# Kernel optimization log

Hardware: AMD Instinct MI355X
Metric: run time of the kernel (lower is better)

## Reference

```python
import jax, jax.numpy as jnp
import numpy as np

H = 14
N = H * H
DIM = 768
INT = 5
LAM = 3.5


def fft_conv_grouped(x, w):
    # x: (B, g*in_c, N) real; w: (g, int_c, in_c, H, H//2+1) complex
    g, int_c, in_c = w.shape[:3]
    B = x.shape[0]
    xf = jnp.fft.rfftn(x.reshape(B, g, in_c, H, H), axes=(-2, -1), norm='ortho')
    yf = jnp.einsum('bgchf,gichf->bgihf', xf, w)
    y = jnp.fft.irfftn(yf, s=(H, H), axes=(-2, -1), norm='ortho')
    return y.reshape(B, g * int_c, N)


def soft(x, t):
    # sign(x) * relu(|x| - t)
    return jnp.sign(x) * jnp.maximum(jnp.abs(x) - t, 0.0)


def batch_norm(x, gamma, beta, eps=1e-5):
    # training-mode BatchNorm1d applied per channel over (B, N); x: (B, N, C)
    m = x.mean(axis=(0, 1))
    v = x.var(axis=(0, 1))
    return (x - m) * jax.lax.rsqrt(v + eps) * gamma + beta


def setup_inputs() -> dict:
    key = jax.random.key(0)
    ks = jax.random.split(key, 8)
    B = 32
    Hf = H // 2 + 1
    # kernel: init randn*0.06, then normalize_parameters()
    kr = jax.random.normal(ks[0], (DIM, INT, 1, H, Hf, 2), dtype=jnp.float32) * 0.06
    kc = kr[..., 0] + 1j * kr[..., 1]
    nrm = jnp.sqrt((jnp.abs(kc) ** 2).sum(axis=(2, 3, 4), keepdims=True) * 2.0 / H ** 2)
    kc = kc / nrm
    kernel = jnp.stack([jnp.real(kc), jnp.imag(kc)], axis=-1)
    # L buffer: update_L(lam=1) -> per-group max singular value of Gram kk
    kk = jnp.einsum('gichf,gjchf->gijhf', kc, jnp.conj(kc))
    sv = np.linalg.svd(np.asarray(jnp.transpose(kk, (0, 3, 4, 1, 2))), compute_uv=False)
    L = jnp.asarray(sv.reshape(DIM, -1).max(axis=-1), dtype=jnp.float32)
    hid = 4 * DIM
    return {
        'x': jax.random.normal(ks[1], (B, N, DIM), dtype=jnp.float32),
        'v_w': jax.random.normal(ks[2], (DIM, DIM), dtype=jnp.float32) * 0.02,
        'proj_w': jax.random.normal(ks[3], (DIM, DIM), dtype=jnp.float32) * 0.02,
        'proj_b': jnp.zeros((DIM,), dtype=jnp.float32),
        'kernel': kernel,
        'kernel2': jax.random.normal(ks[4], (DIM, 1, 1, H, Hf, 2), dtype=jnp.float32) * 0.02,
        'n1_g': jnp.ones((DIM,), dtype=jnp.float32),
        'n1_b': jnp.zeros((DIM,), dtype=jnp.float32),
        'n2_g': jnp.ones((DIM,), dtype=jnp.float32),
        'n2_b': jnp.zeros((DIM,), dtype=jnp.float32),
        'fc1_w': jax.random.normal(ks[5], (hid, DIM), dtype=jnp.float32) * 0.02,
        'fc1_b': jnp.zeros((hid,), dtype=jnp.float32),
        'fc2_w': jax.random.normal(ks[6], (DIM, hid), dtype=jnp.float32) * 0.02,
        'fc2_b': jnp.zeros((DIM,), dtype=jnp.float32),
        'L': L,
    }


def reference(x, v_w, proj_w, proj_b, kernel, kernel2, n1_g, n1_b, n2_g, n2_b, fc1_w, fc1_b, fc2_w, fc2_b, L):
    k = kernel[..., 0] + 1j * kernel[..., 1]                 # (g, int, 1, H, Hf)
    kk = jnp.einsum('gichf,gjchf->gijhf', k, jnp.conj(k))     # (g, int, int, H, Hf)
    vx = x @ v_w.T                                            # v Linear, no bias
    xc = jnp.swapaxes(vx, -2, -1)                             # (B, C, N)
    u = fft_conv_grouped(xc, k)                               # (B, g*int, N)
    Lv = jnp.repeat(L, INT)[None, :, None]                    # (1, g*int, 1)
    # ISTA: init soft-threshold then 3 gradient + shrink steps
    s = soft(u, LAM)
    for _ in range(3):
        s = s - (fft_conv_grouped(s, kk) - u) / Lv
        s = soft(s, LAM / Lv)
    # reconstruct with conjugate-transposed kernel, then mix with kernel2
    new = fft_conv_grouped(s, jnp.swapaxes(jnp.conj(k), 1, 2))  # (B, g, N)
    k2 = kernel2[..., 0] + 1j * kernel2[..., 1]
    new = fft_conv_grouped(new, k2)
    new = jnp.swapaxes(new, -2, -1)                           # (B, N, C)
    new = x + (batch_norm(new, n1_g, n1_b) @ proj_w.T + proj_b)
    h = jax.nn.gelu(batch_norm(new, n2_g, n2_b) @ fc1_w.T + fc1_b, approximate=False)
    return new + (h @ fc2_w.T + fc2_b)
```

## Files before the change

kernel.cpp:

```cpp
#include <hip/hip_runtime.h>
#include <cmath>

typedef unsigned short u16;
typedef __bf16 bf16x8 __attribute__((ext_vector_type(8)));
typedef float f32x4 __attribute__((ext_vector_type(4)));
typedef float float4v __attribute__((ext_vector_type(4)));
typedef u16 ushort4v __attribute__((ext_vector_type(4)));
typedef u16 ushort8v __attribute__((ext_vector_type(8)));

#define DIMC 768
#define NP 196
#define MTOT 6272
#define HIDC 3072
#define LAMC 3.5f

__device__ const float C14d[14] = {
  1.0f, 0.9009688679024191f, 0.6234898018587336f, 0.22252093395631445f,
  -0.22252093395631445f, -0.6234898018587336f, -0.9009688679024191f, -1.0f,
  -0.9009688679024191f, -0.6234898018587336f, -0.22252093395631445f,
  0.22252093395631445f, 0.6234898018587336f, 0.9009688679024191f
};
__device__ const float S14d[14] = {
  0.0f, 0.43388373911755823f, 0.7818314824680298f, 0.9749279121818236f,
  0.9749279121818236f, 0.7818314824680298f, 0.43388373911755823f, 0.0f,
  -0.43388373911755823f, -0.7818314824680298f, -0.9749279121818236f,
  -0.9749279121818236f, -0.7818314824680298f, -0.43388373911755823f
};

__device__ __forceinline__ u16 f2bf(float f) {
  unsigned u = __builtin_bit_cast(unsigned, f);
  unsigned r = u + 0x7FFFu + ((u >> 16) & 1u);
  return (u16)(r >> 16);
}

typedef const __attribute__((address_space(1))) u16* gas_p;
typedef __attribute__((address_space(3))) u16* las_p;
__device__ __forceinline__ void gl16(const u16* g, u16* l) {
  __builtin_amdgcn_global_load_lds((gas_p)g, (las_p)l, 16, 0, 0);
}

__global__ __launch_bounds__(256) void initfg_k(u16* __restrict__ Ff, u16* __restrict__ Gf) {
  int idx = blockIdx.x * 256 + threadIdx.x;
  if (idx < 50176) {
    int j = idx & 7, lane = (idx >> 3) & 63;
    int mk = idx >> 9, k0 = mk % 7, m0 = mk / 7;
    int s = m0 * 16 + (lane & 15);
    int q = k0 * 32 + (lane >> 4) * 8 + j;
    float v = 0.f;
    if (q < 196) {
      int kr = s >> 4, f = (s >> 1) & 7, r = q / 14, c = q % 14;
      int th = (kr * r + f * c) % 14;
      v = (s & 1) ? -S14d[th] : C14d[th];
    }
    Ff[idx] = f2bf(v);
  } else if (idx < 50176 + 46592) {
    int t = idx - 50176;
    int j = t & 7, lane = (t >> 3) & 63;
    int pk = t >> 9, k0 = pk % 7, p0 = pk / 7;
    int p = p0 * 16 + (lane & 15);
    int s = k0 * 32 + (lane >> 4) * 8 + j;
    float v = 0.f;
    if (p < 196) {
      int kr = s >> 4, f = (s >> 1) & 7, r = p / 14, c = p % 14;
      int th = (kr * r + f * c) % 14;
      float w = (f == 0 || f == 7) ? 1.f : 2.f;
      v = (w * (1.f / 196.f)) * ((s & 1) ? -S14d[th] : C14d[th]);
    }
    Gf[t] = f2bf(v);
  }
}

__global__ __launch_bounds__(256) void cvtw2_k(
    const float* __restrict__ w0, const float* __restrict__ w1,
    u16* __restrict__ o0, u16* __restrict__ o1) {
  int idx = blockIdx.x * 256 + threadIdx.x;
  const float* s; u16* d; int base;
  if (idx < 147456) { s = w0; d = o0; base = 0; }
  else              { s = w1; d = o1; base = 147456; }
  int i4 = (idx - base) * 4;
  float4v v = *(const float4v*)(s + i4);
  ushort4v o;
#pragma unroll
  for (int j = 0; j < 4; ++j) o[j] = f2bf(v[j]);
  *(ushort4v*)(d + i4) = o;
}

__global__ __launch_bounds__(256) void cvt4_k(const float* __restrict__ s,
                                              u16* __restrict__ d, int n4) {
  int idx = blockIdx.x * 256 + threadIdx.x;
  if (idx >= n4) return;
  int i4 = idx * 4;
  float4v v = *(const float4v*)(s + i4);
  ushort4v o;
#pragma unroll
  for (int j = 0; j < 4; ++j) o[j] = f2bf(v[j]);
  *(ushort4v*)(d + i4) = o;
}

__global__ __launch_bounds__(256) void scalefc1_k(const float* __restrict__ w,
    const float* __restrict__ sc, u16* __restrict__ d) {
  int idx = blockIdx.x * 256 + threadIdx.x;
  int i4 = idx * 4;
  int k = i4 % DIMC;
  float4v v = *(const float4v*)(w + i4);
  float4v s = *(const float4v*)(sc + k);
  v = v * s;
  ushort4v o;
#pragma unroll
  for (int j = 0; j < 4; ++j) o[j] = f2bf(v[j]);
  *(ushort4v*)(d + i4) = o;
}

__global__ __launch_bounds__(256) void c0_k(const float* __restrict__ projw,
    const float* __restrict__ sh, const float* __restrict__ pb,
    float* __restrict__ c0) {
  int n = blockIdx.x * 256 + threadIdx.x;
  if (n >= DIMC) return;
  const float* row = projw + (size_t)n * DIMC;
  float s = 0.f;
  for (int g = 0; g < DIMC; g += 4) {
    float4v r = *(const float4v*)(row + g);
    float4v h = *(const float4v*)(sh + g);
    s += r[0] * h[0] + r[1] * h[1] + r[2] * h[2] + r[3] * h[3];
  }
  c0[n] = s + pb[n];
}

__global__ __launch_bounds__(256) void d0_k(const float* __restrict__ fc1w,
    const float* __restrict__ sh, const float* __restrict__ fb,
    float* __restrict__ d0) {
  int n = blockIdx.x * 256 + threadIdx.x;
  if (n >= HIDC) return;
  const float* row = fc1w + (size_t)n * DIMC;
  float s = 0.f;
  for (int k = 0; k < DIMC; k += 4) {
    float4v r = *(const float4v*)(row + k);
    float4v h = *(const float4v*)(sh + k);
    s += r[0] * h[0] + r[1] * h[1] + r[2] * h[2] + r[3] * h[3];
  }
  d0[n] = s + fb[n];
}

__global__ __launch_bounds__(256) void base_k(const float* __restrict__ x,
    const float* __restrict__ c0, float* __restrict__ new2,
    u16* __restrict__ new2bf) {
  int idx = blockIdx.x * 256 + threadIdx.x;
  size_t i4 = (size_t)idx * 4;
  int c = (int)(i4 % DIMC);
  float4v v = *(const float4v*)(x + i4);
  float4v a = *(const float4v*)(c0 + c);
  v = v + a;
  *(float4v*)(new2 + i4) = v;
  ushort4v o;
#pragma unroll
  for (int j = 0; j < 4; ++j) o[j] = f2bf(v[j]);
  *(ushort4v*)(new2bf + i4) = o;
}

__global__ __launch_bounds__(64) void tilesum_k(const int* __restrict__ cnt,
    const int* __restrict__ wl, const float* __restrict__ newm,
    float* __restrict__ tsum, float* __restrict__ tsq,
    unsigned* __restrict__ maskg, unsigned* __restrict__ bmask) {
  const int nf = *cnt;
  const int lane = threadIdx.x;
  for (int wi = blockIdx.x; wi < nf; wi += gridDim.x) {
    int tile = wl[wi];
    int g = tile >> 5, b = tile & 31;
    float s = 0.f, q = 0.f;
    for (int m = lane; m < 196; m += 64) {
      float v = newm[((size_t)b * 196 + m) * DIMC + g];
      s += v; q += v * v;
    }
#pragma unroll
    for (int off = 32; off; off >>= 1) { s += __shfl_xor(s, off); q += __shfl_xor(q, off); }
    if (lane == 0) {
      tsum[tile] = s; tsq[tile] = q;
      atomicOr(&maskg[g], 1u << b);
      atomicOr(bmask, 1u << b);
    }
  }
}

__global__ __launch_bounds__(256) void stats1_fin_k(const float* __restrict__ tsum,
    const float* __restrict__ tsq, const unsigned* __restrict__ maskg,
    const float* __restrict__ gam, const float* __restrict__ bet,
    float* __restrict__ scale, float* __restrict__ shift) {
  int c = blockIdx.x * 256 + threadIdx.x;
  if (c >= DIMC) return;
  unsigned mask = maskg[c];
  float S = 0.f, Q = 0.f;
  for (int b = 0; b < 32; ++b)
    if ((mask >> b) & 1) { S += tsum[c * 32 + b]; Q += tsq[c * 32 + b]; }
  float m = S * (1.0f / 6272.0f);
  float v = Q * (1.0f / 6272.0f) - m * m;
  v = fmaxf(v, 0.f);
  float rs = rsqrtf(v + 1e-5f);
  float sc = gam[c] * rs;
  scale[c] = sc;
  shift[c] = bet[c] - m * sc;
}

__global__ __launch_bounds__(256) void corr_k(const unsigned* __restrict__ maskg,
    const unsigned* __restrict__ bmask, const float* __restrict__ newm,
    const float* __restrict__ projw, const float* __restrict__ sc1,
    float* __restrict__ new2, u16* __restrict__ new2bf) {
  const int b = blockIdx.x, t = threadIdx.x;
  if (!((*bmask >> b) & 1)) return;
  __shared__ int gl[768];
  __shared__ int ngs;
  if (t == 0) {
    int n = 0;
    for (int g = 0; g < DIMC; ++g) if ((maskg[g] >> b) & 1) gl[n++] = g;
    ngs = n;
  }
  __syncthreads();
  const int n_g = ngs;
  for (int m = 0; m < 196; ++m) {
    size_t row = ((size_t)b * 196 + m) * DIMC;
    for (int n = t; n < DIMC; n += 256) {
      float a = 0.f;
      for (int i = 0; i < n_g; ++i) {
        int g = gl[i];
        a += sc1[g] * newm[row + g] * projw[(size_t)n * DIMC + g];
      }
      float nv = new2[row + n] + a;
      new2[row + n] = nv;
      new2bf[row + n] = f2bf(nv);
    }
  }
}

template<int EPI>
__global__ __launch_bounds__(256) void gemm_k(
    const u16* __restrict__ A, const u16* __restrict__ Bw,
    const float* __restrict__ bias, const float* __restrict__ res,
    void* __restrict__ Cp, int Nr, int Kr, int ld, int NB) {
  __shared__ __attribute__((aligned(16))) u16 As[128 * 32];
  __shared__ __attribute__((aligned(16))) u16 Bs[128 * 32];
  const int t = threadIdx.x;
  const int wid = t >> 6, lane = t & 63;

  const int bid = blockIdx.x;
  const int xcd = bid & 7, j = bid >> 3;
  const int bmi = xcd + 8 * (j / NB);
  if (bmi >= 49) return;
  const int bn = (j % NB) * 128, bm = bmi * 128;

  const int wm = (wid >> 1) * 64, wn = (wid & 1) * 64;
  const int l15 = lane & 15, l4 = lane >> 4;
  const int srow = lane >> 2, scol = (lane & 3) * 8;

  f32x4 acc[4][4];
#pragma unroll
  for (int a = 0; a < 4; ++a)
#pragma unroll
    for (int b2 = 0; b2 < 4; ++b2) acc[a][b2] = (f32x4){0.f, 0.f, 0.f, 0.f};

  const u16* gA0 = A + (size_t)(bm + wid * 16 + srow) * ld + scol;
  const u16* gB0 = Bw + (size_t)(bn + wid * 16 + srow) * ld + scol;
  u16* lA = As + wid * 512;
  u16* lB = Bs + wid * 512;

  for (int k0 = 0; k0 < Kr; k0 += 32) {
    gl16(gA0 + k0, lA);
    gl16(gA0 + (size_t)64 * ld + k0, lA + 2048);
    gl16(gB0 + k0, lB);
    gl16(gB0 + (size_t)64 * ld + k0, lB + 2048);
    __syncthreads();

    bf16x8 af[4], bfv[4];
#pragma unroll
    for (int mb = 0; mb < 4; ++mb)
      af[mb] = *(const bf16x8*)&As[(wm + mb * 16 + l15) * 32 + l4 * 8];
#pragma unroll
    for (int nb = 0; nb < 4; ++nb)
      bfv[nb] = *(const bf16x8*)&Bs[(wn + nb * 16 + l15) * 32 + l4 * 8];
#pragma unroll
    for (int mb = 0; mb < 4; ++mb)
#pragma unroll
      for (int nb = 0; nb < 4; ++nb)
        acc[mb][nb] = __builtin_amdgcn_mfma_f32_16x16x32_bf16(af[mb], bfv[nb], acc[mb][nb], 0, 0, 0);
    __syncthreads();
  }

#pragma unroll
  for (int mb = 0; mb < 4; ++mb) {
#pragma unroll
    for (int nb = 0; nb < 4; ++nb) {
      int n = bn + wn + nb * 16 + l15;
      if (EPI == 0) {
        int m0 = bm + wm + mb * 16 + l4 * 4;
        int bb = m0 / 196, np0 = m0 - bb * 196;
        *(float4v*)&((float*)Cp)[((size_t)bb * DIMC + n) * 196 + np0] =
            (float4v){acc[mb][nb][0], acc[mb][nb][1], acc[mb][nb][2], acc[mb][nb][3]};
      } else {
#pragma unroll
        for (int r = 0; r < 4; ++r) {
          int m = bm + wm + mb * 16 + l4 * 4 + r;
          float v = acc[mb][nb][r];
          if (EPI == 1) {
            ((float*)Cp)[(size_t)m * Nr + n] = v + bias[n] + res[(size_t)m * Nr + n];
          } else {
            float vb = v + bias[n];
            float ge = 0.5f * vb * (1.f + erff(vb * 0.70710678118654752f));
            ((u16*)Cp)[(size_t)m * Nr + n] = f2bf(ge);
          }
        }
      }
    }
  }
}

__global__ __launch_bounds__(256) void stats_part_k(const float* __restrict__ A,
                                                    float* __restrict__ part) {
  int blk = blockIdx.x, t = threadIdx.x;
  float s0a = 0, s0b = 0, s0c = 0, s1a = 0, s1b = 0, s1c = 0;
  const float* base = A + (size_t)blk * 64 * DIMC;
  for (int r = 0; r < 64; ++r) {
    const float* row = base + (size_t)r * DIMC;
    float v0 = row[t], v1 = row[t + 256], v2 = row[t + 512];
    s0a += v0; s1a += v0 * v0;
    s0b += v1; s1b += v1 * v1;
    s0c += v2; s1c += v2 * v2;
  }
  part[(size_t)blk * DIMC + t] = s0a;
  part[(size_t)blk * DIMC + t + 256] = s0b;
  part[(size_t)blk * DIMC + t + 512] = s0c;
  float* p2 = part + 98 * DIMC;
  p2[(size_t)blk * DIMC + t] = s1a;
  p2[(size_t)blk * DIMC + t + 256] = s1b;
  p2[(size_t)blk * DIMC + t + 512] = s1c;
}

__global__ __launch_bounds__(256) void stats_fin_k(const float* __restrict__ part,
    const float* __restrict__ gam, const float* __restrict__ bet,
    float* __restrict__ scale, float* __restrict__ shift) {
  int c = blockIdx.x * 256 + threadIdx.x;
  if (c >= DIMC) return;
  float S = 0.f, Q = 0.f;
  for (int b = 0; b < 98; ++b) {
    S += part[(size_t)b * DIMC + c];
    Q += part[(size_t)(98 + b) * DIMC + c];
  }
  float m = S * (1.0f / 6272.0f);
  float v = Q * (1.0f / 6272.0f) - m * m;
  v = fmaxf(v, 0.f);
  float rs = rsqrtf(v + 1e-5f);
  float sc = gam[c] * rs;
  scale[c] = sc;
  shift[c] = bet[c] - m * sc;
}

__global__ __launch_bounds__(64) void checkmfma_k(
    const float* __restrict__ vxt, const float* __restrict__ kern,
    const u16* __restrict__ Ff, const u16* __restrict__ Gf,
    int* __restrict__ cnt, int* __restrict__ wl) {
  __shared__ float xf[16 * 228];
  const int lane = threadIdx.x;
  const int wgb = blockIdx.x;
  const int g = wgb >> 1, bhalf = wgb & 1;
  const int tl = lane & 15, h = lane >> 4;
  const float* xbase = vxt + ((size_t)(bhalf * 16 + tl) * DIMC + g) * 196;

  bf16x8 Bx[7];
#pragma unroll
  for (int k0 = 0; k0 < 7; ++k0) {
    int q0 = k0 * 32 + h * 8;
    ushort8v tv;
    if (k0 < 6) {
      float4v f0 = *(const float4v*)(xbase + q0);
      float4v f1 = *(const float4v*)(xbase + q0 + 4);
#pragma unroll
      for (int j = 0; j < 4; ++j) { tv[j] = f2bf(f0[j]); tv[j + 4] = f2bf(f1[j]); }
    } else {
#pragma unroll
      for (int j = 0; j < 8; ++j) {
        int q = q0 + j;
        tv[j] = (q < 196) ? f2bf(xbase[q]) : (u16)0;
      }
    }
    Bx[k0] = __builtin_bit_cast(bf16x8, tv);
  }

  for (int m0 = 0; m0 < 14; ++m0) {
    f32x4 acc = (f32x4){0.f, 0.f, 0.f, 0.f};
#pragma unroll
    for (int k0 = 0; k0 < 7; ++k0) {
      bf16x8 Af = __builtin_bit_cast(bf16x8,
          *(const ushort8v*)(Ff + ((size_t)(m0 * 7 + k0) * 64 + lane) * 8));
      acc = __builtin_amdgcn_mfma_f32_16x16x32_bf16(Af, Bx[k0], acc, 0, 0, 0);
    }
    *(f32x4*)&xf[tl * 228 + m0 * 16 + h * 4] = acc;
  }

  bf16x8 By[5][7];
#pragma unroll
  for (int i = 0; i < 5; ++i) {
    const float* kb = kern + ((size_t)g * 5 + i) * 224;
#pragma unroll
    for (int k0 = 0; k0 < 7; ++k0) {
      f32x4 x0 = *(const f32x4*)&xf[tl * 228 + k0 * 32 + h * 8];
      f32x4 x1 = *(const f32x4*)&xf[tl * 228 + k0 * 32 + h * 8 + 4];
      int mb = k0 * 16 + h * 4;
      float2 ka = *(const float2*)(kb + (mb + 0) * 2);
      float2 kc = *(const float2*)(kb + (mb + 1) * 2);
      float2 ke = *(const float2*)(kb + (mb + 2) * 2);
      float2 kg = *(const float2*)(kb + (mb + 3) * 2);
      ushort8v tv;
      tv[0] = f2bf(ka.x * x0[0] - ka.y * x0[1]);
      tv[1] = f2bf(ka.x * x0[1] + ka.y * x0[0]);
      tv[2] = f2bf(kc.x * x0[2] - kc.y * x0[3]);
      tv[3] = f2bf(kc.x * x0[3] + kc.y * x0[2]);
      tv[4] = f2bf(ke.x * x1[0] - ke.y * x1[1]);
      tv[5] = f2bf(ke.x * x1[1] + ke.y * x1[0]);
      tv[6] = f2bf(kg.x * x1[2] - kg.y * x1[3]);
      tv[7] = f2bf(kg.x * x1[3] + kg.y * x1[2]);
      By[i][k0] = __builtin_bit_cast(bf16x8, tv);
    }
  }

  float vmax = 0.f;
  for (int p0 = 0; p0 < 13; ++p0) {
    f32x4 a0 = (f32x4){0.f, 0.f, 0.f, 0.f};
    f32x4 a1 = a0, a2 = a0, a3 = a0, a4 = a0;
#pragma unroll
    for (int k0 = 0; k0 < 7; ++k0) {
      bf16x8 Ag = __builtin_bit_cast(bf16x8,
          *(const ushort8v*)(Gf + ((size_t)(p0 * 7 + k0) * 64 + lane) * 8));
      a0 = __builtin_amdgcn_mfma_f32_16x16x32_bf16(Ag, By[0][k0], a0, 0, 0, 0);
      a1 = __builtin_amdgcn_mfma_f32_16x16x32_bf16(Ag, By[1][k0], a1, 0, 0, 0);
      a2 = __builtin_amdgcn_mfma_f32_16x16x32_bf16(Ag, By[2][k0], a2, 0, 0, 0);
      a3 = __builtin_amdgcn_mfma_f32_16x16x32_bf16(Ag, By[3][k0], a3, 0, 0, 0);
      a4 = __builtin_amdgcn_mfma_f32_16x16x32_bf16(Ag, By[4][k0], a4, 0, 0, 0);
    }
#pragma unroll
    for (int r = 0; r < 4; ++r) {
      vmax = fmaxf(vmax, fabsf(a0[r]));
      vmax = fmaxf(vmax, fabsf(a1[r]));
      vmax = fmaxf(vmax, fabsf(a2[r]));
      vmax = fmaxf(vmax, fabsf(a3[r]));
      vmax = fmaxf(vmax, fabsf(a4[r]));
    }
  }
  vmax = fmaxf(vmax, __shfl_xor(vmax, 16));
  vmax = fmaxf(vmax, __shfl_xor(vmax, 32));
  if (lane < 16 && vmax > (LAMC - 0.1f)) {
    int idx = atomicAdd(cnt, 1);
    wl[idx] = g * 32 + bhalf * 16 + lane;
  }
}

__global__ __launch_bounds__(64) void slow_k(
    const float* __restrict__ vxt, const float* __restrict__ kern,
    const float* __restrict__ kern2, const float* __restrict__ Lbuf,
    const int* __restrict__ cnt, const int* __restrict__ wl,
    float* __restrict__ outp) {
  const int t = threadIdx.x;
  __shared__ float TC[196], TSn[196];
  __shared__ float xs[196];
  __shared__ float t1R[112], t1I[112];
  __shared__ float t2R[112], t2I[112];
  __shared__ float zr[112], zi[112];
  __shared__ float kR[5][112], kI[5][112];
  __shared__ float uu[5][196];
  __shared__ float ss[5][196];
  __shared__ float k2R[112], k2I[112];

  for (int i = t; i < 196; i += 64) {
    int a = i / 14, c = i - (i / 14) * 14;
    int m = (a * c) % 14;
    TC[i] = C14d[m]; TSn[i] = S14d[m];
  }
  const int ntile = *cnt;

  auto rowsFwd = [&](const float* xsrc) {
    for (int i = t; i < 112; i += 64) {
      int r = i >> 3, f = i & 7;
      const float* xp = xsrc + r * 14;
      const float* tc = &TC[f * 14]; const float* tsn = &TSn[f * 14];
      float ar = 0.f, ai = 0.f;
#pragma unroll
      for (int c = 0; c < 14; ++c) { float xv = xp[c]; ar += xv * tc[c]; ai -= xv * tsn[c]; }
      t1R[i] = ar; t1I[i] = ai;
    }
    __syncthreads();
  };
  auto colsFwd = [&](float* oR, float* oI) {
    for (int i = t; i < 112; i += 64) {
      int kr = i >> 3, f = i & 7;
      const float* tc = &TC[kr * 14]; const float* tsn = &TSn[kr * 14];
      float br = 0.f, bi = 0.f;
#pragma unroll
      for (int r = 0; r < 14; ++r) {
        float xr = t1R[r * 8 + f], xi = t1I[r * 8 + f];
        br += tc[r] * xr + tsn[r] * xi;
        bi += tc[r] * xi - tsn[r] * xr;
      }
      oR[i] = br; oI[i] = bi;
    }
    __syncthreads();
  };
  auto colsInv = [&]() {
    for (int i = t; i < 112; i += 64) {
      int r = i >> 3, f = i & 7;
      const float* tc = &TC[r * 14]; const float* tsn = &TSn[r * 14];
      float br = 0.f, bi = 0.f;
#pragma unroll
      for (int kr = 0; kr < 14; ++kr) {
        float xr = t1R[kr * 8 + f], xi = t1I[kr * 8 + f];
        br += tc[kr] * xr - tsn[kr] * xi;
        bi += tc[kr] * xi + tsn[kr] * xr;
      }
      t2R[i] = br; t2I[i] = bi;
    }
    __syncthreads();
  };
  auto rowVal = [&](int r, int c) -> float {
    const float* pR = &t2R[r * 8]; const float* pI = &t2I[r * 8];
    float v = pR[0] + ((c & 1) ? -pR[7] : pR[7]);
    float s2 = 0.f;
#pragma unroll
    for (int f = 1; f < 7; ++f) s2 += pR[f] * TC[f * 14 + c] - pI[f] * TSn[f * 14 + c];
    return (v + 2.f * s2) * (1.0f / 196.0f);
  };

  for (int widx = blockIdx.x; widx < ntile; widx += gridDim.x) {
    const int tile = wl[widx];
    const int g = tile >> 5, b = tile & 31;
    __syncthreads();
    for (int i = t; i < 560; i += 64) {
      int ii = i / 112, p = i - ii * 112;
      const float* kp = kern + ((size_t)g * 5 + ii) * 224 + p * 2;
      kR[ii][p] = kp[0]; kI[ii][p] = kp[1];
    }
    for (int i = t; i < 196; i += 64) xs[i] = vxt[((size_t)b * DIMC + g) * 196 + i];
    for (int i = t; i < 112; i += 64) {
      k2R[i] = kern2[(size_t)g * 224 + i * 2];
      k2I[i] = kern2[(size_t)g * 224 + i * 2 + 1];
    }
    __syncthreads();

    rowsFwd(xs);
    colsFwd(zr, zi);
    for (int ii = 0; ii < 5; ++ii) {
      for (int i = t; i < 112; i += 64) {
        float a = kR[ii][i], b2 = kI[ii][i];
        t1R[i] = a * zr[i] - b2 * zi[i];
        t1I[i] = a * zi[i] + b2 * zr[i];
      }
      __syncthreads();
      colsInv();
      for (int i = t; i < 196; i += 64) uu[ii][i] = rowVal(i / 14, i - (i / 14) * 14);
      __syncthreads();
    }

    const float invL = 1.0f / Lbuf[g];
    const float thr = LAMC * invL;
    {
      float* up = &uu[0][0];
      float* sp = &ss[0][0];
      for (int i = t; i < 980; i += 64) {
        float v = up[i];
        float a = fabsf(v) - LAMC;
        sp[i] = a > 0.f ? copysignf(a, v) : 0.f;
      }
    }
    __syncthreads();

    for (int iter = 0; iter < 4; ++iter) {
      for (int i = t; i < 112; i += 64) { zr[i] = 0.f; zi[i] = 0.f; }
      __syncthreads();
      for (int ii = 0; ii < 5; ++ii) {
        rowsFwd(&ss[ii][0]);
        colsFwd(t2R, t2I);
        for (int i = t; i < 112; i += 64) {
          float a = kR[ii][i], b2 = kI[ii][i];
          zr[i] += a * t2R[i] + b2 * t2I[i];
          zi[i] += a * t2I[i] - b2 * t2R[i];
        }
        __syncthreads();
      }
      if (iter == 3) break;
      for (int ii = 0; ii < 5; ++ii) {
        for (int i = t; i < 112; i += 64) {
          float a = kR[ii][i], b2 = kI[ii][i];
          t1R[i] = a * zr[i] - b2 * zi[i];
          t1I[i] = a * zi[i] + b2 * zr[i];
        }
        __syncthreads();
        colsInv();
        for (int i = t; i < 196; i += 64) {
          float v = rowVal(i / 14, i - (i / 14) * 14);
          float sv = ss[ii][i] - (v - uu[ii][i]) * invL;
          float aa = fabsf(sv) - thr;
          ss[ii][i] = aa > 0.f ? copysignf(aa, sv) : 0.f;
        }
        __syncthreads();
      }
    }

    if (t < 28) {
      int kr = t >> 1, f = (t & 1) * 7;
      int d = kr * 8 + f;
      int srci = ((14 - kr) % 14) * 8 + f;
      float pr = 0.5f * (zr[d] + zr[srci]);
      float pi = 0.5f * (zi[d] - zi[srci]);
      zr[d] = pr; zi[d] = pi;
    }
    __syncthreads();
    for (int i = t; i < 112; i += 64) {
      float a = k2R[i], b2 = k2I[i];
      t1R[i] = a * zr[i] - b2 * zi[i];
      t1I[i] = a * zi[i] + b2 * zr[i];
    }
    __syncthreads();
    colsInv();
    for (int i = t; i < 196; i += 64)
      outp[((size_t)(b * 196 + i)) * DIMC + g] = rowVal(i / 14, i - (i / 14) * 14);
  }
}

extern "C" void kernel_launch(void* const* d_in, const int* in_sizes, int n_in,
                              void* d_out, int out_size, void* d_ws, size_t ws_size,
                              hipStream_t stream) {
  (void)in_sizes; (void)n_in; (void)out_size;
  const float* x      = (const float*)d_in[0];
  const float* v_w    = (const float*)d_in[1];
  const float* proj_w = (const float*)d_in[2];
  const float* proj_b = (const float*)d_in[3];
  const float* kern   = (const float*)d_in[4];
  const float* kern2  = (const float*)d_in[5];
  const float* n1g    = (const float*)d_in[6];
  const float* n1b    = (const float*)d_in[7];
  const float* n2g    = (const float*)d_in[8];
  const float* n2b    = (const float*)d_in[9];
  const float* fc1w   = (const float*)d_in[10];
  const float* fc1b   = (const float*)d_in[11];
  const float* fc2w   = (const float*)d_in[12];
  const float* fc2b   = (const float*)d_in[13];
  const float* Lb     = (const float*)d_in[14];
  float* out = (float*)d_out;

  char* ws = (char*)d_ws;
  size_t o = 0;
  auto alloc = [&](size_t bytes) { size_t r = o; o += (bytes + 255) & ~(size_t)255; return r; };
  u16*   vwbf   = (u16*)(ws + alloc(589824 * 2));
  u16*   fc2bf  = (u16*)(ws + alloc(2359296 * 2));
  u16*   fc1s   = (u16*)(ws + alloc(2359296 * 2));
  u16*   Ffb    = (u16*)(ws + alloc(50176 * 2));
  u16*   Gfb    = (u16*)(ws + alloc(46592 * 2));
  float* sc1    = (float*)(ws + alloc(768 * 4));
  float* sh1    = (float*)(ws + alloc(768 * 4));
  float* sc2    = (float*)(ws + alloc(768 * 4));
  float* sh2    = (float*)(ws + alloc(768 * 4));
  float* c0     = (float*)(ws + alloc(768 * 4));
  float* d0     = (float*)(ws + alloc(3072 * 4));
  float* part   = (float*)(ws + alloc(98 * 768 * 2 * 4));
  char*  zblk   = (char*)(ws + alloc(4096));
  int*      cnt   = (int*)zblk;
  unsigned* bmask = (unsigned*)(zblk + 4);
  unsigned* maskg = (unsigned*)(zblk + 8);
  int*   wl     = (int*)(ws + alloc(24576 * 4));
  float* tsum   = (float*)(ws + alloc(24576 * 4));
  float* tsq    = (float*)(ws + alloc(24576 * 4));
  u16*   xbf    = (u16*)(ws + alloc((size_t)MTOT * DIMC * 2));
  u16*   n2bf   = (u16*)(ws + alloc((size_t)MTOT * DIMC * 2));
  float* vxt    = (float*)(ws + alloc((size_t)MTOT * DIMC * 4));
  float* newm   = (float*)(ws + alloc((size_t)MTOT * DIMC * 4));
  float* new2   = (float*)(ws + alloc((size_t)MTOT * DIMC * 4));
  u16*   hbf    = (u16*)vxt;
  if (ws_size < o) return;

  hipMemsetAsync(zblk, 0, 4096, stream);

  initfg_k<<<378, 256, 0, stream>>>(Ffb, Gfb);
  cvtw2_k<<<2880, 256, 0, stream>>>(v_w, fc2w, vwbf, fc2bf);
  cvt4_k<<<4704, 256, 0, stream>>>(x, xbf, 1204224);

  gemm_k<0><<<336, 256, 0, stream>>>(xbf, vwbf, nullptr, nullptr, vxt, DIMC, DIMC, DIMC, 6);
  checkmfma_k<<<1536, 64, 0, stream>>>(vxt, kern, Ffb, Gfb, cnt, wl);
  slow_k<<<1024, 64, 0, stream>>>(vxt, kern, kern2, Lb, cnt, wl, newm);
  tilesum_k<<<256, 64, 0, stream>>>(cnt, wl, newm, tsum, tsq, maskg, bmask);
  stats1_fin_k<<<3, 256, 0, stream>>>(tsum, tsq, maskg, n1g, n1b, sc1, sh1);
  c0_k<<<3, 256, 0, stream>>>(proj_w, sh1, proj_b, c0);
  base_k<<<4704, 256, 0, stream>>>(x, c0, new2, n2bf);
  corr_k<<<32, 256, 0, stream>>>(maskg, bmask, newm, proj_w, sc1, new2, n2bf);
  stats_part_k<<<98, 256, 0, stream>>>(new2, part);
  stats_fin_k<<<3, 256, 0, stream>>>(part, n2g, n2b, sc2, sh2);
  d0_k<<<12, 256, 0, stream>>>(fc1w, sh2, fc1b, d0);
  scalefc1_k<<<2304, 256, 0, stream>>>(fc1w, sc2, fc1s);
  gemm_k<2><<<1344, 256, 0, stream>>>(n2bf, fc1s, d0, nullptr, hbf, HIDC, DIMC, DIMC, 24);
  gemm_k<1><<<336, 256, 0, stream>>>(hbf, fc2bf, fc2b, new2, out, DIMC, HIDC, HIDC, 6);
}
```

Before: 324.2 us.

## Fuse prep, stats, correction and fc1-folding kernels to cut launches

Merges the three conversion/init kernels into one prep kernel and folds the per-tile sum and sum-of-squares into slow_k. It also fuses the BN1 stats with the c0 projection, and the base add with the sparse correction and BN2 partial sums into a 2D-grid kernel. d0 and the fc1 scaling are merged into one kernel. This cuts launch count and drops a full re-read of new2 for statistics, and it replaces the 32-block serial correction kernel with a 896-block version. The cost is a larger partials buffer and a serial 896-term reduction per channel in stats2fin_k.

```diff
diff --git a/kernel.cpp b/kernel.cpp
--- a/kernel.cpp
+++ b/kernel.cpp
@@ -39,194 +39,60 @@
   __builtin_amdgcn_global_load_lds((gas_p)g, (las_p)l, 16, 0, 0);
 }
 
-__global__ __launch_bounds__(256) void initfg_k(u16* __restrict__ Ff, u16* __restrict__ Gf) {
-  int idx = blockIdx.x * 256 + threadIdx.x;
-  if (idx < 50176) {
-    int j = idx & 7, lane = (idx >> 3) & 63;
-    int mk = idx >> 9, k0 = mk % 7, m0 = mk / 7;
-    int s = m0 * 16 + (lane & 15);
-    int q = k0 * 32 + (lane >> 4) * 8 + j;
-    float v = 0.f;
-    if (q < 196) {
-      int kr = s >> 4, f = (s >> 1) & 7, r = q / 14, c = q % 14;
-      int th = (kr * r + f * c) % 14;
-      v = (s & 1) ? -S14d[th] : C14d[th];
-    }
-    Ff[idx] = f2bf(v);
-  } else if (idx < 50176 + 46592) {
-    int t = idx - 50176;
-    int j = t & 7, lane = (t >> 3) & 63;
-    int pk = t >> 9, k0 = pk % 7, p0 = pk / 7;
-    int p = p0 * 16 + (lane & 15);
-    int s = k0 * 32 + (lane >> 4) * 8 + j;
-    float v = 0.f;
-    if (p < 196) {
-      int kr = s >> 4, f = (s >> 1) & 7, r = p / 14, c = p % 14;
-      int th = (kr * r + f * c) % 14;
-      float w = (f == 0 || f == 7) ? 1.f : 2.f;
-      v = (w * (1.f / 196.f)) * ((s & 1) ? -S14d[th] : C14d[th]);
-    }
-    Gf[t] = f2bf(v);
-  }
-}
-
-__global__ __launch_bounds__(256) void cvtw2_k(
-    const float* __restrict__ w0, const float* __restrict__ w1,
-    u16* __restrict__ o0, u16* __restrict__ o1) {
-  int idx = blockIdx.x * 256 + threadIdx.x;
-  const float* s; u16* d; int base;
-  if (idx < 147456) { s = w0; d = o0; base = 0; }
-  else              { s = w1; d = o1; base = 147456; }
-  int i4 = (idx - base) * 4;
-  float4v v = *(const float4v*)(s + i4);
-  ushort4v o;
-#pragma unroll
-  for (int j = 0; j < 4; ++j) o[j] = f2bf(v[j]);
-  *(ushort4v*)(d + i4) = o;
-}
-
-__global__ __launch_bounds__(256) void cvt4_k(const float* __restrict__ s,
-                                              u16* __restrict__ d, int n4) {
-  int idx = blockIdx.x * 256 + threadIdx.x;
-  if (idx >= n4) return;
-  int i4 = idx * 4;
-  float4v v = *(const float4v*)(s + i4);
-  ushort4v o;
-#pragma unroll
-  for (int j = 0; j < 4; ++j) o[j] = f2bf(v[j]);
-  *(ushort4v*)(d + i4) = o;
-}
-
-__global__ __launch_bounds__(256) void scalefc1_k(const float* __restrict__ w,
-    const float* __restrict__ sc, u16* __restrict__ d) {
-  int idx = blockIdx.x * 256 + threadIdx.x;
-  int i4 = idx * 4;
-  int k = i4 % DIMC;
-  float4v v = *(const float4v*)(w + i4);
-  float4v s = *(const float4v*)(sc + k);
-  v = v * s;
-  ushort4v o;
-#pragma unroll
-  for (int j = 0; j < 4; ++j) o[j] = f2bf(v[j]);
-  *(ushort4v*)(d + i4) = o;
-}
-
-__global__ __launch_bounds__(256) void c0_k(const float* __restrict__ projw,
-    const float* __restrict__ sh, const float* __restrict__ pb,
-    float* __restrict__ c0) {
-  int n = blockIdx.x * 256 + threadIdx.x;
-  if (n >= DIMC) return;
-  const float* row = projw + (size_t)n * DIMC;
-  float s = 0.f;
-  for (int g = 0; g < DIMC; g += 4) {
-    float4v r = *(const float4v*)(row + g);
-    float4v h = *(const float4v*)(sh + g);
-    s += r[0] * h[0] + r[1] * h[1] + r[2] * h[2] + r[3] * h[3];
-  }
-  c0[n] = s + pb[n];
-}
-
-__global__ __launch_bounds__(256) void d0_k(const float* __restrict__ fc1w,
-    const float* __restrict__ sh, const float* __restrict__ fb,
-    float* __restrict__ d0) {
-  int n = blockIdx.x * 256 + threadIdx.x;
-  if (n >= HIDC) return;
-  const float* row = fc1w + (size_t)n * DIMC;
-  float s = 0.f;
-  for (int k = 0; k < DIMC; k += 4) {
-    float4v r = *(const float4v*)(row + k);
-    float4v h = *(const float4v*)(sh + k);
-    s += r[0] * h[0] + r[1] * h[1] + r[2] * h[2] + r[3] * h[3];
-  }
-  d0[n] = s + fb[n];
-}
-
-__global__ __launch_bounds__(256) void base_k(const float* __restrict__ x,
-    const float* __restrict__ c0, float* __restrict__ new2,
-    u16* __restrict__ new2bf) {
-  int idx = blockIdx.x * 256 + threadIdx.x;
-  size_t i4 = (size_t)idx * 4;
-  int c = (int)(i4 % DIMC);
-  float4v v = *(const float4v*)(x + i4);
-  float4v a = *(const float4v*)(c0 + c);
-  v = v + a;
-  *(float4v*)(new2 + i4) = v;
-  ushort4v o;
-#pragma unroll
-  for (int j = 0; j < 4; ++j) o[j] = f2bf(v[j]);
-  *(ushort4v*)(new2bf + i4) = o;
-}
-
-__global__ __launch_bounds__(64) void tilesum_k(const int* __restrict__ cnt,
-    const int* __restrict__ wl, const float* __restrict__ newm,
-    float* __restrict__ tsum, float* __restrict__ tsq,
-    unsigned* __restrict__ maskg, unsigned* __restrict__ bmask) {
-  const int nf = *cnt;
-  const int lane = threadIdx.x;
-  for (int wi = blockIdx.x; wi < nf; wi += gridDim.x) {
-    int tile = wl[wi];
-    int g = tile >> 5, b = tile & 31;
-    float s = 0.f, q = 0.f;
-    for (int m = lane; m < 196; m += 64) {
-      float v = newm[((size_t)b * 196 + m) * DIMC + g];
-      s += v; q += v * v;
-    }
-#pragma unroll
-    for (int off = 32; off; off >>= 1) { s += __shfl_xor(s, off); q += __shfl_xor(q, off); }
-    if (lane == 0) {
-      tsum[tile] = s; tsq[tile] = q;
-      atomicOr(&maskg[g], 1u << b);
-      atomicOr(bmask, 1u << b);
-    }
-  }
-}
-
-__global__ __launch_bounds__(256) void stats1_fin_k(const float* __restrict__ tsum,
-    const float* __restrict__ tsq, const unsigned* __restrict__ maskg,
-    const float* __restrict__ gam, const float* __restrict__ bet,
-    float* __restrict__ scale, float* __restrict__ shift) {
-  int c = blockIdx.x * 256 + threadIdx.x;
-  if (c >= DIMC) return;
-  unsigned mask = maskg[c];
-  float S = 0.f, Q = 0.f;
-  for (int b = 0; b < 32; ++b)
-    if ((mask >> b) & 1) { S += tsum[c * 32 + b]; Q += tsq[c * 32 + b]; }
-  float m = S * (1.0f / 6272.0f);
-  float v = Q * (1.0f / 6272.0f) - m * m;
-  v = fmaxf(v, 0.f);
-  float rs = rsqrtf(v + 1e-5f);
-  float sc = gam[c] * rs;
-  scale[c] = sc;
-  shift[c] = bet[c] - m * sc;
-}
-
-__global__ __launch_bounds__(256) void corr_k(const unsigned* __restrict__ maskg,
-    const unsigned* __restrict__ bmask, const float* __restrict__ newm,
-    const float* __restrict__ projw, const float* __restrict__ sc1,
-    float* __restrict__ new2, u16* __restrict__ new2bf) {
-  const int b = blockIdx.x, t = threadIdx.x;
-  if (!((*bmask >> b) & 1)) return;
-  __shared__ int gl[768];
-  __shared__ int ngs;
-  if (t == 0) {
-    int n = 0;
-    for (int g = 0; g < DIMC; ++g) if ((maskg[g] >> b) & 1) gl[n++] = g;
-    ngs = n;
-  }
-  __syncthreads();
-  const int n_g = ngs;
-  for (int m = 0; m < 196; ++m) {
-    size_t row = ((size_t)b * 196 + m) * DIMC;
-    for (int n = t; n < DIMC; n += 256) {
-      float a = 0.f;
-      for (int i = 0; i < n_g; ++i) {
-        int g = gl[i];
-        a += sc1[g] * newm[row + g] * projw[(size_t)n * DIMC + g];
-      }
-      float nv = new2[row + n] + a;
-      new2[row + n] = nv;
-      new2bf[row + n] = f2bf(nv);
-    }
+__global__ __launch_bounds__(256) void prep_k(
+    const float* __restrict__ v_w, const float* __restrict__ fc2w,
+    const float* __restrict__ x,
+    u16* __restrict__ vwbf, u16* __restrict__ fc2bf, u16* __restrict__ xbf,
+    u16* __restrict__ Ff, u16* __restrict__ Gf) {
+  const int bid = blockIdx.x, t = threadIdx.x;
+  if (bid < 378) {
+    int idx = bid * 256 + t;
+    if (idx < 50176) {
+      int j = idx & 7, lane = (idx >> 3) & 63;
+      int mk = idx >> 9, k0 = mk % 7, m0 = mk / 7;
+      int s = m0 * 16 + (lane & 15);
+      int q = k0 * 32 + (lane >> 4) * 8 + j;
+      float v = 0.f;
+      if (q < 196) {
+        int kr = s >> 4, f = (s >> 1) & 7, r = q / 14, c = q % 14;
+        int th = (kr * r + f * c) % 14;
+        v = (s & 1) ? -S14d[th] : C14d[th];
+      }
+      Ff[idx] = f2bf(v);
+    } else {
+      int t2 = idx - 50176;
+      int j = t2 & 7, lane = (t2 >> 3) & 63;
+      int pk = t2 >> 9, k0 = pk % 7, p0 = pk / 7;
+      int p = p0 * 16 + (lane & 15);
+      int s = k0 * 32 + (lane >> 4) * 8 + j;
+      float v = 0.f;
+      if (p < 196) {
+        int kr = s >> 4, f = (s >> 1) & 7, r = p / 14, c = p % 14;
+        int th = (kr * r + f * c) % 14;
+        float w = (f == 0 || f == 7) ? 1.f : 2.f;
+        v = (w * (1.f / 196.f)) * ((s & 1) ? -S14d[th] : C14d[th]);
+      }
+      Gf[t2] = f2bf(v);
+    }
+  } else if (bid < 3258) {
+    int idx = (bid - 378) * 256 + t;
+    const float* s; u16* d; int base;
+    if (idx < 147456) { s = v_w; d = vwbf; base = 0; }
+    else              { s = fc2w; d = fc2bf; base = 147456; }
+    int i4 = (idx - base) * 4;
+    float4v v = *(const float4v*)(s + i4);
+    ushort4v o;
+#pragma unroll
+    for (int j = 0; j < 4; ++j) o[j] = f2bf(v[j]);
+    *(ushort4v*)(d + i4) = o;
+  } else {
+    int idx = (bid - 3258) * 256 + t;
+    int i4 = idx * 4;
+    float4v v = *(const float4v*)(x + i4);
+    ushort4v o;
+#pragma unroll
+    for (int j = 0; j < 4; ++j) o[j] = f2bf(v[j]);
+    *(ushort4v*)(xbf + i4) = o;
   }
 }
 
@@ -309,46 +175,6 @@
       }
     }
   }
-}
-
-__global__ __launch_bounds__(256) void stats_part_k(const float* __restrict__ A,
-                                                    float* __restrict__ part) {
-  int blk = blockIdx.x, t = threadIdx.x;
-  float s0a = 0, s0b = 0, s0c = 0, s1a = 0, s1b = 0, s1c = 0;
-  const float* base = A + (size_t)blk * 64 * DIMC;
-  for (int r = 0; r < 64; ++r) {
-    const float* row = base + (size_t)r * DIMC;
-    float v0 = row[t], v1 = row[t + 256], v2 = row[t + 512];
-    s0a += v0; s1a += v0 * v0;
-    s0b += v1; s1b += v1 * v1;
-    s0c += v2; s1c += v2 * v2;
-  }
-  part[(size_t)blk * DIMC + t] = s0a;
-  part[(size_t)blk * DIMC + t + 256] = s0b;
-  part[(size_t)blk * DIMC + t + 512] = s0c;
-  float* p2 = part + 98 * DIMC;
-  p2[(size_t)blk * DIMC + t] = s1a;
-  p2[(size_t)blk * DIMC + t + 256] = s1b;
-  p2[(size_t)blk * DIMC + t + 512] = s1c;
-}
-
-__global__ __launch_bounds__(256) void stats_fin_k(const float* __restrict__ part,
-    const float* __restrict__ gam, const float* __restrict__ bet,
-    float* __restrict__ scale, float* __restrict__ shift) {
-  int c = blockIdx.x * 256 + threadIdx.x;
-  if (c >= DIMC) return;
-  float S = 0.f, Q = 0.f;
-  for (int b = 0; b < 98; ++b) {
-    S += part[(size_t)b * DIMC + c];
-    Q += part[(size_t)(98 + b) * DIMC + c];
-  }
-  float m = S * (1.0f / 6272.0f);
-  float v = Q * (1.0f / 6272.0f) - m * m;
-  v = fmaxf(v, 0.f);
-  float rs = rsqrtf(v + 1e-5f);
-  float sc = gam[c] * rs;
-  scale[c] = sc;
-  shift[c] = bet[c] - m * sc;
 }
 
 __global__ __launch_bounds__(64) void checkmfma_k(
@@ -454,7 +280,11 @@
     const float* __restrict__ vxt, const float* __restrict__ kern,
     const float* __restrict__ kern2, const float* __restrict__ Lbuf,
     const int* __restrict__ cnt, const int* __restrict__ wl,
-    float* __restrict__ outp) {
+    float* __restrict__ outp,
+    float* __restrict__ tsum, float* __restrict__ tsq,
+    unsigned* __restrict__ maskg, unsigned* __restrict__ bmask) {
+  const int ntile = *cnt;
+  if ((int)blockIdx.x >= ntile) return;
   const int t = threadIdx.x;
   __shared__ float TC[196], TSn[196];
   __shared__ float xs[196];
@@ -471,7 +301,6 @@
     int m = (a * c) % 14;
     TC[i] = C14d[m]; TSn[i] = S14d[m];
   }
-  const int ntile = *cnt;
 
   auto rowsFwd = [&](const float* xsrc) {
     for (int i = t; i < 112; i += 64) {
@@ -615,8 +444,150 @@
     }
     __syncthreads();
     colsInv();
-    for (int i = t; i < 196; i += 64)
-      outp[((size_t)(b * 196 + i)) * DIMC + g] = rowVal(i / 14, i - (i / 14) * 14);
+    float sacc = 0.f, qacc = 0.f;
+    for (int i = t; i < 196; i += 64) {
+      float v = rowVal(i / 14, i - (i / 14) * 14);
+      outp[((size_t)(b * 196 + i)) * DIMC + g] = v;
+      sacc += v; qacc += v * v;
+    }
+#pragma unroll
+    for (int off = 32; off; off >>= 1) {
+      sacc += __shfl_xor(sacc, off);
+      qacc += __shfl_xor(qacc, off);
+    }
+    if (t == 0) {
+      tsum[tile] = sacc; tsq[tile] = qacc;
+      atomicOr(&maskg[g], 1u << b);
+      atomicOr(bmask, 1u << b);
+    }
+  }
+}
+
+__global__ __launch_bounds__(256) void stats1c0_k(
+    const float* __restrict__ tsum, const float* __restrict__ tsq,
+    const unsigned* __restrict__ maskg,
+    const float* __restrict__ gam, const float* __restrict__ bet,
+    const float* __restrict__ projw, const float* __restrict__ pb,
+    float* __restrict__ sc1, float* __restrict__ c0) {
+  __shared__ float sh1s[768];
+  const int t = threadIdx.x;
+  for (int c = t; c < DIMC; c += 256) {
+    unsigned mask = maskg[c];
+    float S = 0.f, Q = 0.f;
+    if (mask) {
+      for (int b = 0; b < 32; ++b)
+        if ((mask >> b) & 1) { S += tsum[c * 32 + b]; Q += tsq[c * 32 + b]; }
+    }
+    float m = S * (1.0f / 6272.0f);
+    float v = fmaxf(Q * (1.0f / 6272.0f) - m * m, 0.f);
+    float rs = rsqrtf(v + 1e-5f);
+    float sc = gam[c] * rs;
+    sh1s[c] = bet[c] - m * sc;
+    if (blockIdx.x == 0) sc1[c] = sc;
+  }
+  __syncthreads();
+  int n = blockIdx.x * 256 + t;
+  const float* row = projw + (size_t)n * DIMC;
+  float s = 0.f;
+  for (int g = 0; g < DIMC; g += 4) {
+    float4v r = *(const float4v*)(row + g);
+    s += r[0] * sh1s[g] + r[1] * sh1s[g + 1] + r[2] * sh1s[g + 2] + r[3] * sh1s[g + 3];
+  }
+  c0[n] = s + pb[n];
+}
+
+__global__ __launch_bounds__(256) void bnb_k(
+    const float* __restrict__ x, const float* __restrict__ c0,
+    const float* __restrict__ sc1, const unsigned* __restrict__ maskg,
+    const unsigned* __restrict__ bmask, const float* __restrict__ newm,
+    const float* __restrict__ projw,
+    float* __restrict__ new2, u16* __restrict__ n2bf,
+    float* __restrict__ part) {
+  const int jb = blockIdx.x, b = blockIdx.y, t = threadIdx.x;
+  __shared__ unsigned gm[24];
+  __shared__ float c0s[768];
+  const bool hasb = ((*bmask >> b) & 1u) != 0u;
+  if (t < 24) {
+    unsigned w = 0;
+    if (hasb)
+      for (int j2 = 0; j2 < 32; ++j2) w |= ((maskg[t * 32 + j2] >> b) & 1u) << j2;
+    gm[t] = w;
+  }
+  for (int c = t; c < 768; c += 256) c0s[c] = c0[c];
+  __syncthreads();
+
+  float S0 = 0, S1 = 0, S2 = 0, Q0 = 0, Q1 = 0, Q2 = 0;
+  for (int mr = 0; mr < 7; ++mr) {
+    size_t row = ((size_t)b * 196 + jb * 7 + mr) * DIMC;
+#pragma unroll
+    for (int j2 = 0; j2 < 3; ++j2) {
+      int n = t + j2 * 256;
+      float v = x[row + n] + c0s[n];
+      if (hasb) {
+        for (int w = 0; w < 24; ++w) {
+          unsigned bits = gm[w];
+          while (bits) {
+            int g = w * 32 + __builtin_ctz(bits);
+            bits &= bits - 1;
+            v += sc1[g] * newm[row + g] * projw[(size_t)n * DIMC + g];
+          }
+        }
+      }
+      new2[row + n] = v;
+      n2bf[row + n] = f2bf(v);
+      if (j2 == 0) { S0 += v; Q0 += v * v; }
+      else if (j2 == 1) { S1 += v; Q1 += v * v; }
+      else { S2 += v; Q2 += v * v; }
+    }
+  }
+  float* p = part + (size_t)(b * 28 + jb) * 1536;
+  p[t] = S0; p[t + 256] = S1; p[t + 512] = S2;
+  p[768 + t] = Q0; p[768 + 256 + t] = Q1; p[768 + 512 + t] = Q2;
+}
+
+__global__ __launch_bounds__(256) void stats2fin_k(const float* __restrict__ part,
+    const float* __restrict__ gam, const float* __restrict__ bet,
+    float* __restrict__ scale, float* __restrict__ shift) {
+  int c = blockIdx.x * 256 + threadIdx.x;
+  float S = 0.f, Q = 0.f;
+  for (int bid = 0; bid < 896; ++bid) {
+    S += part[(size_t)bid * 1536 + c];
+    Q += part[(size_t)bid * 1536 + 768 + c];
+  }
+  float m = S * (1.0f / 6272.0f);
+  float v = fmaxf(Q * (1.0f / 6272.0f) - m * m, 0.f);
+  float rs = rsqrtf(v + 1e-5f);
+  float sc = gam[c] * rs;
+  scale[c] = sc;
+  shift[c] = bet[c] - m * sc;
+}
+
+__global__ __launch_bounds__(256) void foldfc1_k(const float* __restrict__ fc1w,
+    const float* __restrict__ fc1b, const float* __restrict__ sc2,
+    const float* __restrict__ sh2, u16* __restrict__ fc1s,
+    float* __restrict__ d0) {
+  const int bid = blockIdx.x, t = threadIdx.x;
+  if (bid < 12) {
+    int n = bid * 256 + t;
+    const float* row = fc1w + (size_t)n * DIMC;
+    float s = 0.f;
+    for (int k = 0; k < DIMC; k += 4) {
+      float4v r = *(const float4v*)(row + k);
+      float4v h = *(const float4v*)(sh2 + k);
+      s += r[0] * h[0] + r[1] * h[1] + r[2] * h[2] + r[3] * h[3];
+    }
+    d0[n] = s + fc1b[n];
+  } else {
+    int idx = (bid - 12) * 256 + t;
+    int i4 = idx * 4;
+    int k = i4 % DIMC;
+    float4v v = *(const float4v*)(fc1w + i4);
+    float4v s = *(const float4v*)(sc2 + k);
+    v = v * s;
+    ushort4v o;
+#pragma unroll
+    for (int j = 0; j < 4; ++j) o[j] = f2bf(v[j]);
+    *(ushort4v*)(fc1s + i4) = o;
   }
 }
 
@@ -650,12 +621,11 @@
   u16*   Ffb    = (u16*)(ws + alloc(50176 * 2));
   u16*   Gfb    = (u16*)(ws + alloc(46592 * 2));
   float* sc1    = (float*)(ws + alloc(768 * 4));
-  float* sh1    = (float*)(ws + alloc(768 * 4));
   float* sc2    = (float*)(ws + alloc(768 * 4));
   float* sh2    = (float*)(ws + alloc(768 * 4));
   float* c0     = (float*)(ws + alloc(768 * 4));
   float* d0     = (float*)(ws + alloc(3072 * 4));
-  float* part   = (float*)(ws + alloc(98 * 768 * 2 * 4));
+  float* part   = (float*)(ws + alloc((size_t)896 * 1536 * 4));
   char*  zblk   = (char*)(ws + alloc(4096));
   int*      cnt   = (int*)zblk;
   unsigned* bmask = (unsigned*)(zblk + 4);
@@ -673,22 +643,16 @@
 
   hipMemsetAsync(zblk, 0, 4096, stream);
 
-  initfg_k<<<378, 256, 0, stream>>>(Ffb, Gfb);
-  cvtw2_k<<<2880, 256, 0, stream>>>(v_w, fc2w, vwbf, fc2bf);
-  cvt4_k<<<4704, 256, 0, stream>>>(x, xbf, 1204224);
-
+  prep_k<<<7962, 256, 0, stream>>>(v_w, fc2w, x, vwbf, fc2bf, xbf, Ffb, Gfb);
   gemm_k<0><<<336, 256, 0, stream>>>(xbf, vwbf, nullptr, nullptr, vxt, DIMC, DIMC, DIMC, 6);
   checkmfma_k<<<1536, 64, 0, stream>>>(vxt, kern, Ffb, Gfb, cnt, wl);
-  slow_k<<<1024, 64, 0, stream>>>(vxt, kern, kern2, Lb, cnt, wl, newm);
-  tilesum_k<<<256, 64, 0, stream>>>(cnt, wl, newm, tsum, tsq, maskg, bmask);
-  stats1_fin_k<<<3, 256, 0, stream>>>(tsum, tsq, maskg, n1g, n1b, sc1, sh1);
-  c0_k<<<3, 256, 0, stream>>>(proj_w, sh1, proj_b, c0);
-  base_k<<<4704, 256, 0, stream>>>(x, c0, new2, n2bf);
-  corr_k<<<32, 256, 0, stream>>>(maskg, bmask, newm, proj_w, sc1, new2, n2bf);
-  stats_part_k<<<98, 256, 0, stream>>>(new2, part);
-  stats_fin_k<<<3, 256, 0, stream>>>(part, n2g, n2b, sc2, sh2);
-  d0_k<<<12, 256, 0, stream>>>(fc1w, sh2, fc1b, d0);
-  scalefc1_k<<<2304, 256, 0, stream>>>(fc1w, sc2, fc1s);
+  slow_k<<<1024, 64, 0, stream>>>(vxt, kern, kern2, Lb, cnt, wl, newm,
+                                  tsum, tsq, maskg, bmask);
+  stats1c0_k<<<3, 256, 0, stream>>>(tsum, tsq, maskg, n1g, n1b, proj_w, proj_b, sc1, c0);
+  bnb_k<<<dim3(28, 32), 256, 0, stream>>>(x, c0, sc1, maskg, bmask, newm, proj_w,
+                                          new2, n2bf, part);
+  stats2fin_k<<<3, 256, 0, stream>>>(part, n2g, n2b, sc2, sh2);
+  foldfc1_k<<<2316, 256, 0, stream>>>(fc1w, fc1b, sc2, sh2, fc1s, d0);
   gemm_k<2><<<1344, 256, 0, stream>>>(n2bf, fc1s, d0, nullptr, hbf, HIDC, DIMC, DIMC, 24);
   gemm_k<1><<<336, 256, 0, stream>>>(hbf, fc2bf, fc2b, new2, out, DIMC, HIDC, HIDC, 6);
 }
```

Result: slower. 356.6 us (+10.0%).
